# Kernel optimization log

Hardware: AMD Instinct MI355X
Metric: run time of the kernel (lower is better)

## Reference

```python
import jax, jax.numpy as jnp
import numpy as np
import math

D = 128          # domain_size (cells per side)
CELL = 0.1       # cell_size
PS = 0.1         # particle_size
KN = 6.0e6       # spring stiffness
_ALPHA = -math.log(0.5) / math.pi
_GAMMA = _ALPHA / math.sqrt(_ALPHA ** 2 + 1.0)
PM = 4.0 / 3.0 * 3.1415 * CELL ** 3 * 2700.0   # particle_mass
ETA = 2.0 * _GAMMA * math.sqrt(KN * PM)          # damping_coefficient_Eta
DT = 1e-4
EPS = 1e-4       # torch.clamp(dist, 0.0001)

# all 125 roll shifts (k-2, j-2, i-2) applied to dims (2,3,4) of a (1,1,D,D,D) field
SHIFTS = jnp.array([[k - 2, j - 2, i - 2]
                    for i in range(5) for j in range(5) for k in range(5)], dtype=jnp.int32)


def _roll3(a, sh):
    return jnp.roll(a, (sh[0], sh[1], sh[2]), axis=(2, 3, 4))


def _collision(n, xg, yg, zg, vx, vy, vz):
    """Accumulate spring-damper contact force on layer n from both layers over 125 offsets."""
    xn, yn, zn = xg[n], yg[n], zg[n]
    vxn, vyn, vzn = vx[n], vy[n], vz[n]

    def body(carry, sh):
        fx, fy, fz = carry
        for m in range(2):  # the two particle layers (diff*1 / diff*2 in the torch code)
            dx = xn - _roll3(xg[m], sh)
            dy = yn - _roll3(yg[m], sh)
            dz = zn - _roll3(zg[m], sh)
            # tiny floor inside sqrt keeps the self-offset (dist=0) finite; force there is 0 either way
            dist = jnp.sqrt(jnp.maximum(dx * dx + dy * dy + dz * dz, 1e-12))
            dc = jnp.maximum(dist, EPS)
            dvn = ((vxn - _roll3(vx[m], sh)) * dx
                   + (vyn - _roll3(vy[m], sh)) * dy
                   + (vzn - _roll3(vz[m], sh)) * dz) / dc
            # spring + normal damping, gated by overlap (dist < particle_size)
            coef = jnp.where(dist < PS, (KN * (dist - PS) + ETA * dvn) / dc, 0.0)
            fx = fx + coef * dx
            fy = fy + coef * dy
            fz = fz + coef * dz
        return (fx, fy, fz), None

    z0 = jnp.zeros((1, 1, D, D, D), jnp.float32)
    (fx, fy, fz), _ = jax.lax.scan(body, (z0, z0, z0), SHIFTS)
    return fx, fy, fz


def _boundary(p, v, m):
    lo = ((p > PS) & (p < 1.5 * PS)).astype(p.dtype)
    hi = (p > D * CELL - 0.5 * PS - CELL).astype(p.dtype)
    return (KN * lo * m * (1.5 * PS - p)
            - KN * hi * m * (p - D * CELL + CELL + 0.5 * PS)
            - ETA * v * lo * m - ETA * v * hi * m)


def _forward(x_grid, y_grid, z_grid, vx_grid, vy_grid, vz_grid, mask):
    vx, vy, vz = vx_grid, vy_grid, vz_grid
    # sequential over n: layer n=1's collision pass sees layer 0's already-updated
    # velocities, matching the in-place updates of the torch code
    for n in range(2):
        fx, fy, fz = _collision(n, x_grid, y_grid, z_grid, vx, vy, vz)
        fxb = _boundary(x_grid[n], vx[n], mask[n])
        fyb = _boundary(y_grid[n], vy[n], mask[n])
        fzb = _boundary(z_grid[n], vz[n], mask[n])
        vx = vx.at[n].set(vx[n] + DT / PM * mask[n] * (-fx + fxb))
        vy = vy.at[n].set(vy[n] + DT / PM * mask[n] * (-fy + fyb))
        vz = vz.at[n].set(vz[n] + DT / PM * mask[n] * (-9.8 * PM - fz + fzb))
    return jnp.stack([vx, vy, vz])  # (3, 2, 1, 1, D, D, D) updated velocities


def setup_inputs() -> dict:
    key = jax.random.key(0)
    ks = jax.random.split(key, 7)
    shape = (2, 1, 1, D, D, D)
    c = jnp.arange(D, dtype=jnp.float32) * CELL
    # particle position = cell corner + uniform jitter -> realistic contacts (dist < PS)
    x_grid = c[None, None, None, None, None, :] + jax.random.uniform(ks[0], shape, jnp.float32) * CELL
    y_grid = c[None, None, None, None, :, None] + jax.random.uniform(ks[1], shape, jnp.float32) * CELL
    z_grid = c[None, None, None, :, None, None] + jax.random.uniform(ks[2], shape, jnp.float32) * CELL
    vx_grid = 0.1 * jax.random.normal(ks[3], shape, jnp.float32)
    vy_grid = 0.1 * jax.random.normal(ks[4], shape, jnp.float32)
    vz_grid = 0.1 * jax.random.normal(ks[5], shape, jnp.float32)
    mask = (jax.random.uniform(ks[6], shape) < 0.5).astype(jnp.float32)  # cell occupancy
    return {"x_grid": x_grid, "y_grid": y_grid, "z_grid": z_grid,
            "vx_grid": vx_grid, "vy_grid": vy_grid, "vz_grid": vz_grid, "mask": mask}


def reference(x_grid, y_grid, z_grid, vx_grid, vy_grid, vz_grid, mask):
    return _forward(x_grid, y_grid, z_grid, vx_grid, vy_grid, vz_grid, mask)
```

## Files before the change

### kernel.cpp

```cpp
#include <hip/hip_runtime.h>
#include <math.h>

namespace {

constexpr int DD = 128;
constexpr int DM = 127;
constexpr int D3 = DD * DD * DD;

struct Consts {
  float kn, ps, eta, dtpm, grav;
  float lo_hi;
  float hi_th;
  float dcell;
  float cell;
  float hps;
  float ps2;
  float nknps;
};

__device__ inline float bforce(float p, float v, float mkv, const Consts& c) {
  float lo = ((p > c.ps) && (p < c.lo_hi)) ? mkv : 0.0f;
  float hi = (p > c.hi_th) ? mkv : 0.0f;
  float t = ((p - c.dcell) + c.cell) + c.hps;
  return c.kn * lo * (c.lo_hi - p) - c.kn * hi * t - c.eta * v * lo - c.eta * v * hi;
}

__device__ __forceinline__ float f4c(const float4& v, int u) {
  return u == 0 ? v.x : (u == 1 ? v.y : (u == 2 ? v.z : v.w));
}

template <int R>
__device__ void collide(int x, int y, int z,
                        const float* __restrict__ xg, const float* __restrict__ yg,
                        const float* __restrict__ zg,
                        const float* __restrict__ v0x, const float* __restrict__ v0y,
                        const float* __restrict__ v0z,
                        const float* __restrict__ v1x, const float* __restrict__ v1y,
                        const float* __restrict__ v1z,
                        float xn, float yn, float zn,
                        float vxn, float vyn, float vzn,
                        float& fx, float& fy, float& fz, const Consts& c) {
  int xw[2 * R + 1];
#pragma unroll
  for (int ox = -R; ox <= R; ++ox) xw[ox + R] = (x + ox) & DM;

  for (int oz = -R; oz <= R; ++oz) {
    const int zr = (z + oz) & DM;
    for (int oy = -R; oy <= R; ++oy) {
      const int yr = (y + oy) & DM;
      const int rb = (zr * DD + yr) * DD;
#pragma unroll
      for (int m = 0; m < 2; ++m) {
        const float* __restrict__ PX = xg + m * D3 + rb;
        const float* __restrict__ PY = yg + m * D3 + rb;
        const float* __restrict__ PZ = zg + m * D3 + rb;
        const float* __restrict__ VX = (m == 0 ? v0x : v1x) + rb;
        const float* __restrict__ VY = (m == 0 ? v0y : v1y) + rb;
        const float* __restrict__ VZ = (m == 0 ? v0z : v1z) + rb;
#pragma unroll
        for (int ox = -R; ox <= R; ++ox) {
          const int xi = xw[ox + R];
          float dx = xn - PX[xi];
          float dy = yn - PY[xi];
          float dz = zn - PZ[xi];
          float d2 = fmaf(dx, dx, fmaf(dy, dy, dz * dz));
          float d2c = fmaxf(d2, 1e-12f);
          float r = __builtin_amdgcn_rsqf(d2c);
          float dist = d2c * r;
          float inv = fminf(r, 1.0e4f);
          float dvx = vxn - VX[xi];
          float dvy = vyn - VY[xi];
          float dvz = vzn - VZ[xi];
          float dvn = fmaf(dvx, dx, fmaf(dvy, dy, dvz * dz)) * inv;
          float coef = (dist < c.ps) ? (fmaf(c.kn, dist - c.ps, c.eta * dvn) * inv) : 0.0f;
          fx = fmaf(coef, dx, fx);
          fy = fmaf(coef, dy, fy);
          fz = fmaf(coef, dz, fz);
        }
      }
    }
  }
}

__global__ void __launch_bounds__(256)
checker(const float* __restrict__ xg, const float* __restrict__ yg,
        const float* __restrict__ zg, unsigned* flag, float cell) {
  int i = blockIdx.x * 256 + threadIdx.x;
  int ix = i & DM;
  int iy = (i >> 7) & DM;
  int iz = (i >> 14) & DM;
  float jx = xg[i] - ix * cell;
  float jy = yg[i] - iy * cell;
  float jz = zg[i] - iz * cell;
  const float lo = -1e-5f, hi = cell + 1e-5f;
  bool bad = (jx < lo) | (jx > hi) | (jy < lo) | (jy > hi) | (jz < lo) | (jz > hi);
  if (bad) atomicOr(flag, 1u);
}

__global__ void __launch_bounds__(256)
dem_pass(int n,
         const float* __restrict__ xg, const float* __restrict__ yg,
         const float* __restrict__ zg,
         const float* __restrict__ v0x, const float* __restrict__ v0y,
         const float* __restrict__ v0z,
         const float* __restrict__ v1x, const float* __restrict__ v1y,
         const float* __restrict__ v1z,
         const float* __restrict__ vnx, const float* __restrict__ vny,
         const float* __restrict__ vnz,
         const float* __restrict__ maskn,
         float* __restrict__ outx, float* __restrict__ outy, float* __restrict__ outz,
         const unsigned* __restrict__ flag, Consts cc) {
  const int t = threadIdx.x;
  const int tx = t & 31;
  const int ty = t >> 5;
  const int wg = blockIdx.x;
  const int id = ((wg & 7) << 8) | (wg >> 3);
  const int z = id >> 4;
  const int y = ((id & 15) << 3) | ty;
  const int x0 = tx << 2;
  const int idx = (z * DD + y) * DD + x0;
  const int nn = n * D3;

  const float4 xc4 = *(const float4*)(xg + nn + idx);
  const float4 yc4 = *(const float4*)(yg + nn + idx);
  const float4 zc4 = *(const float4*)(zg + nn + idx);
  const float4 vx4 = *(const float4*)(vnx + idx);
  const float4 vy4 = *(const float4*)(vny + idx);
  const float4 vz4 = *(const float4*)(vnz + idx);
  const float4 mk4 = *(const float4*)(maskn + idx);

  float pxc[4] = {xc4.x, xc4.y, xc4.z, xc4.w};
  float pyc[4] = {yc4.x, yc4.y, yc4.z, yc4.w};
  float pzc[4] = {zc4.x, zc4.y, zc4.z, zc4.w};
  float vxc[4] = {vx4.x, vx4.y, vx4.z, vx4.w};
  float vyc[4] = {vy4.x, vy4.y, vy4.z, vy4.w};
  float vzc[4] = {vz4.x, vz4.y, vz4.z, vz4.w};
  float mkc[4] = {mk4.x, mk4.y, mk4.z, mk4.w};

  float fxA[4] = {0.f, 0.f, 0.f, 0.f};
  float fyA[4] = {0.f, 0.f, 0.f, 0.f};
  float fzA[4] = {0.f, 0.f, 0.f, 0.f};

  if (*flag == 0u) {
    const int laneL = (t & 32) | ((tx + 31) & 31);
    const int laneR = (t & 32) | ((tx + 1) & 31);
    const float* __restrict__ Q0[6] = {xg, yg, zg, v0x, v0y, v0z};
    const float* __restrict__ Q1[6] = {xg + D3, yg + D3, zg + D3, v1x, v1y, v1z};

    const float KNc = cc.kn, PS2 = cc.ps2, NKNPS = cc.nknps, ETAc = cc.eta;

    auto compute_row = [&](const float4 (&Bf)[6]) {
      float lo[6], hi[6];
#pragma unroll
      for (int f = 0; f < 6; ++f) {
        lo[f] = __shfl(Bf[f].w, laneL, 64);
        hi[f] = __shfl(Bf[f].x, laneR, 64);
      }
#pragma unroll
      for (int i = 0; i < 4; ++i) {
#pragma unroll
        for (int ox = 0; ox < 3; ++ox) {
          const int u = i + ox - 1;
          const float wx  = (u < 0) ? lo[0] : ((u > 3) ? hi[0] : f4c(Bf[0], u));
          const float wy  = (u < 0) ? lo[1] : ((u > 3) ? hi[1] : f4c(Bf[1], u));
          const float wz  = (u < 0) ? lo[2] : ((u > 3) ? hi[2] : f4c(Bf[2], u));
          const float wvx = (u < 0) ? lo[3] : ((u > 3) ? hi[3] : f4c(Bf[3], u));
          const float wvy = (u < 0) ? lo[4] : ((u > 3) ? hi[4] : f4c(Bf[4], u));
          const float wvz = (u < 0) ? lo[5] : ((u > 3) ? hi[5] : f4c(Bf[5], u));
          float dx = pxc[i] - wx;
          float dy = pyc[i] - wy;
          float dz = pzc[i] - wz;
          float d2 = fmaf(dx, dx, fmaf(dy, dy, dz * dz));
          float r = __builtin_amdgcn_rsqf(d2);
          float inv = fminf(r, 1.0e4f);
          float inv2 = inv * inv;
          float dvx = vxc[i] - wvx;
          float dvy = vyc[i] - wvy;
          float dvz = vzc[i] - wvz;
          float dvnr = fmaf(dvx, dx, fmaf(dvy, dy, dvz * dz));
          float coef = fmaf(ETAc, dvnr * inv2, fmaf(NKNPS, inv, KNc));
          coef = (d2 < PS2) ? coef : 0.0f;
          fxA[i] = fmaf(coef, dx, fxA[i]);
          fyA[i] = fmaf(coef, dy, fyA[i]);
          fzA[i] = fmaf(coef, dz, fzA[i]);
        }
      }
    };

    float4 A[6], B[6];
    {
      const int rb0 = (((z + DM) & DM) * DD + ((y + DM) & DM)) * DD + x0;
#pragma unroll
      for (int f = 0; f < 6; ++f) A[f] = *(const float4*)(Q0[f] + rb0);
    }

#pragma unroll 1
    for (int k = 0; k < 9; ++k) {
      const int iz = (k * 11) >> 5;
      const int iy = k - iz * 3;
      const int rb = (((z + iz + DM) & DM) * DD + ((y + iy + DM) & DM)) * DD + x0;
#pragma unroll
      for (int f = 0; f < 6; ++f) B[f] = *(const float4*)(Q1[f] + rb);
      compute_row(A);
      const int k1 = (k < 8) ? k + 1 : 8;
      const int iz1 = (k1 * 11) >> 5;
      const int iy1 = k1 - iz1 * 3;
      const int rb1 = (((z + iz1 + DM) & DM) * DD + ((y + iy1 + DM) & DM)) * DD + x0;
#pragma unroll
      for (int f = 0; f < 6; ++f) A[f] = *(const float4*)(Q0[f] + rb1);
      compute_row(B);
    }
  } else {
#pragma unroll
    for (int i = 0; i < 4; ++i) {
      collide<2>(x0 + i, y, z, xg, yg, zg, v0x, v0y, v0z, v1x, v1y, v1z,
                 pxc[i], pyc[i], pzc[i], vxc[i], vyc[i], vzc[i],
                 fxA[i], fyA[i], fzA[i], cc);
    }
  }

  float4 ox4, oy4, oz4;
#pragma unroll
  for (int i = 0; i < 4; ++i) {
    const float fxb = bforce(pxc[i], vxc[i], mkc[i], cc);
    const float fyb = bforce(pyc[i], vyc[i], mkc[i], cc);
    const float fzb = bforce(pzc[i], vzc[i], mkc[i], cc);
    const float s = cc.dtpm * mkc[i];
    (&ox4.x)[i] = vxc[i] + s * (fxb - fxA[i]);
    (&oy4.x)[i] = vyc[i] + s * (fyb - fyA[i]);
    (&oz4.x)[i] = vzc[i] + s * ((cc.grav - fzA[i]) + fzb);
  }
  *(float4*)(outx + idx) = ox4;
  *(float4*)(outy + idx) = oy4;
  *(float4*)(outz + idx) = oz4;
}

}

extern "C" void kernel_launch(void* const* d_in, const int* in_sizes, int n_in,
                              void* d_out, int out_size, void* d_ws, size_t ws_size,
                              hipStream_t stream) {
  const float* xg = (const float*)d_in[0];
  const float* yg = (const float*)d_in[1];
  const float* zg = (const float*)d_in[2];
  const float* vx = (const float*)d_in[3];
  const float* vy = (const float*)d_in[4];
  const float* vz = (const float*)d_in[5];
  const float* mk = (const float*)d_in[6];
  float* out = (float*)d_out;
  unsigned* flag = (unsigned*)d_ws;

  const double PSd = 0.1, CELLd = 0.1, KNd = 6.0e6;
  const double ALPHA = -log(0.5) / 3.141592653589793;
  const double GAMMA = ALPHA / sqrt(ALPHA * ALPHA + 1.0);
  const double PMd = 4.0 / 3.0 * 3.1415 * (0.1 * 0.1 * 0.1) * 2700.0;
  const double ETAd = 2.0 * GAMMA * sqrt(KNd * PMd);

  Consts cc;
  cc.kn = (float)KNd;
  cc.ps = (float)PSd;
  cc.eta = (float)ETAd;
  cc.dtpm = (float)(1e-4 / PMd);
  cc.grav = (float)(-9.8 * PMd);
  cc.lo_hi = (float)(1.5 * PSd);
  cc.hi_th = (float)(DD * CELLd - 0.5 * PSd - CELLd);
  cc.dcell = (float)(DD * CELLd);
  cc.cell = (float)CELLd;
  cc.hps = (float)(0.5 * PSd);
  cc.ps2 = cc.ps * cc.ps;
  cc.nknps = -(cc.kn * cc.ps);

  hipMemsetAsync(d_ws, 0, sizeof(unsigned), stream);
  checker<<<(2 * D3) / 256, 256, 0, stream>>>(xg, yg, zg, flag, cc.cell);

  dim3 blk(256, 1, 1), grd(2048, 1, 1);
  dem_pass<<<grd, blk, 0, stream>>>(
      0, xg, yg, zg,
      vx, vy, vz,
      vx + D3, vy + D3, vz + D3,
      vx, vy, vz,
      mk,
      out, out + 2 * D3, out + 4 * D3,
      flag, cc);
  dem_pass<<<grd, blk, 0, stream>>>(
      1, xg, yg, zg,
      out, out + 2 * D3, out + 4 * D3,
      vx + D3, vy + D3, vz + D3,
      vx + D3, vy + D3, vz + D3,
      mk + D3,
      out + D3, out + 3 * D3, out + 5 * D3,
      flag, cc);
}
```

Before: 192.5 us.

## Register-block two y-rows per thread to share neighbor row loads

Each thread now computes two adjacent y rows instead of one. It walks 12 neighbor rows (3 z by 4 y) instead of 9 and applies each loaded row to both output rows where it is in range. This cuts global and L2 loads per output from 9 rows to 6, and the grid is halved to match. The cost is more live registers, which may lower occupancy, and half as many workgroups.

```diff
diff --git a/kernel.cpp b/kernel.cpp
--- a/kernel.cpp
+++ b/kernel.cpp
@@ -114,32 +114,36 @@
   const int tx = t & 31;
   const int ty = t >> 5;
   const int wg = blockIdx.x;
-  const int id = ((wg & 7) << 8) | (wg >> 3);
-  const int z = id >> 4;
-  const int y = ((id & 15) << 3) | ty;
+  const int id = ((wg & 7) << 7) | (wg >> 3);
+  const int z = id >> 3;
+  const int y0 = ((id & 7) << 4) | (ty << 1);
   const int x0 = tx << 2;
-  const int idx = (z * DD + y) * DD + x0;
+  const int idx0 = (z * DD + y0) * DD + x0;
+  const int idx1 = idx0 + DD;
   const int nn = n * D3;
 
-  const float4 xc4 = *(const float4*)(xg + nn + idx);
-  const float4 yc4 = *(const float4*)(yg + nn + idx);
-  const float4 zc4 = *(const float4*)(zg + nn + idx);
-  const float4 vx4 = *(const float4*)(vnx + idx);
-  const float4 vy4 = *(const float4*)(vny + idx);
-  const float4 vz4 = *(const float4*)(vnz + idx);
-  const float4 mk4 = *(const float4*)(maskn + idx);
-
-  float pxc[4] = {xc4.x, xc4.y, xc4.z, xc4.w};
-  float pyc[4] = {yc4.x, yc4.y, yc4.z, yc4.w};
-  float pzc[4] = {zc4.x, zc4.y, zc4.z, zc4.w};
-  float vxc[4] = {vx4.x, vx4.y, vx4.z, vx4.w};
-  float vyc[4] = {vy4.x, vy4.y, vy4.z, vy4.w};
-  float vzc[4] = {vz4.x, vz4.y, vz4.z, vz4.w};
-  float mkc[4] = {mk4.x, mk4.y, mk4.z, mk4.w};
-
-  float fxA[4] = {0.f, 0.f, 0.f, 0.f};
-  float fyA[4] = {0.f, 0.f, 0.f, 0.f};
-  float fzA[4] = {0.f, 0.f, 0.f, 0.f};
+  float px0[4], py0[4], pz0[4], vx0[4], vy0[4], vz0[4], mk0[4];
+  float px1[4], py1[4], pz1[4], vx1[4], vy1[4], vz1[4], mk1[4];
+  {
+    float4 a;
+    a = *(const float4*)(xg + nn + idx0);  px0[0]=a.x; px0[1]=a.y; px0[2]=a.z; px0[3]=a.w;
+    a = *(const float4*)(yg + nn + idx0);  py0[0]=a.x; py0[1]=a.y; py0[2]=a.z; py0[3]=a.w;
+    a = *(const float4*)(zg + nn + idx0);  pz0[0]=a.x; pz0[1]=a.y; pz0[2]=a.z; pz0[3]=a.w;
+    a = *(const float4*)(vnx + idx0);      vx0[0]=a.x; vx0[1]=a.y; vx0[2]=a.z; vx0[3]=a.w;
+    a = *(const float4*)(vny + idx0);      vy0[0]=a.x; vy0[1]=a.y; vy0[2]=a.z; vy0[3]=a.w;
+    a = *(const float4*)(vnz + idx0);      vz0[0]=a.x; vz0[1]=a.y; vz0[2]=a.z; vz0[3]=a.w;
+    a = *(const float4*)(maskn + idx0);    mk0[0]=a.x; mk0[1]=a.y; mk0[2]=a.z; mk0[3]=a.w;
+    a = *(const float4*)(xg + nn + idx1);  px1[0]=a.x; px1[1]=a.y; px1[2]=a.z; px1[3]=a.w;
+    a = *(const float4*)(yg + nn + idx1);  py1[0]=a.x; py1[1]=a.y; py1[2]=a.z; py1[3]=a.w;
+    a = *(const float4*)(zg + nn + idx1);  pz1[0]=a.x; pz1[1]=a.y; pz1[2]=a.z; pz1[3]=a.w;
+    a = *(const float4*)(vnx + idx1);      vx1[0]=a.x; vx1[1]=a.y; vx1[2]=a.z; vx1[3]=a.w;
+    a = *(const float4*)(vny + idx1);      vy1[0]=a.x; vy1[1]=a.y; vy1[2]=a.z; vy1[3]=a.w;
+    a = *(const float4*)(vnz + idx1);      vz1[0]=a.x; vz1[1]=a.y; vz1[2]=a.z; vz1[3]=a.w;
+    a = *(const float4*)(maskn + idx1);    mk1[0]=a.x; mk1[1]=a.y; mk1[2]=a.z; mk1[3]=a.w;
+  }
+
+  float fx0[4] = {0.f,0.f,0.f,0.f}, fy0[4] = {0.f,0.f,0.f,0.f}, fz0[4] = {0.f,0.f,0.f,0.f};
+  float fx1[4] = {0.f,0.f,0.f,0.f}, fy1[4] = {0.f,0.f,0.f,0.f}, fz1[4] = {0.f,0.f,0.f,0.f};
 
   if (*flag == 0u) {
     const int laneL = (t & 32) | ((tx + 31) & 31);
@@ -149,90 +153,116 @@
 
     const float KNc = cc.kn, PS2 = cc.ps2, NKNPS = cc.nknps, ETAc = cc.eta;
 
-    auto compute_row = [&](const float4 (&Bf)[6]) {
-      float lo[6], hi[6];
-#pragma unroll
-      for (int f = 0; f < 6; ++f) {
-        lo[f] = __shfl(Bf[f].w, laneL, 64);
-        hi[f] = __shfl(Bf[f].x, laneR, 64);
-      }
+    auto interact4 = [&](const float4 (&Rf)[6], const float (&lo)[6], const float (&hi)[6],
+                         const float (&px)[4], const float (&py)[4], const float (&pz)[4],
+                         const float (&vx)[4], const float (&vy)[4], const float (&vz)[4],
+                         float (&fx)[4], float (&fy)[4], float (&fz)[4]) {
 #pragma unroll
       for (int i = 0; i < 4; ++i) {
 #pragma unroll
         for (int ox = 0; ox < 3; ++ox) {
           const int u = i + ox - 1;
-          const float wx  = (u < 0) ? lo[0] : ((u > 3) ? hi[0] : f4c(Bf[0], u));
-          const float wy  = (u < 0) ? lo[1] : ((u > 3) ? hi[1] : f4c(Bf[1], u));
-          const float wz  = (u < 0) ? lo[2] : ((u > 3) ? hi[2] : f4c(Bf[2], u));
-          const float wvx = (u < 0) ? lo[3] : ((u > 3) ? hi[3] : f4c(Bf[3], u));
-          const float wvy = (u < 0) ? lo[4] : ((u > 3) ? hi[4] : f4c(Bf[4], u));
-          const float wvz = (u < 0) ? lo[5] : ((u > 3) ? hi[5] : f4c(Bf[5], u));
-          float dx = pxc[i] - wx;
-          float dy = pyc[i] - wy;
-          float dz = pzc[i] - wz;
+          const float wx  = (u < 0) ? lo[0] : ((u > 3) ? hi[0] : f4c(Rf[0], u));
+          const float wy  = (u < 0) ? lo[1] : ((u > 3) ? hi[1] : f4c(Rf[1], u));
+          const float wz  = (u < 0) ? lo[2] : ((u > 3) ? hi[2] : f4c(Rf[2], u));
+          const float wvx = (u < 0) ? lo[3] : ((u > 3) ? hi[3] : f4c(Rf[3], u));
+          const float wvy = (u < 0) ? lo[4] : ((u > 3) ? hi[4] : f4c(Rf[4], u));
+          const float wvz = (u < 0) ? lo[5] : ((u > 3) ? hi[5] : f4c(Rf[5], u));
+          float dx = px[i] - wx;
+          float dy = py[i] - wy;
+          float dz = pz[i] - wz;
           float d2 = fmaf(dx, dx, fmaf(dy, dy, dz * dz));
           float r = __builtin_amdgcn_rsqf(d2);
           float inv = fminf(r, 1.0e4f);
           float inv2 = inv * inv;
-          float dvx = vxc[i] - wvx;
-          float dvy = vyc[i] - wvy;
-          float dvz = vzc[i] - wvz;
+          float dvx = vx[i] - wvx;
+          float dvy = vy[i] - wvy;
+          float dvz = vz[i] - wvz;
           float dvnr = fmaf(dvx, dx, fmaf(dvy, dy, dvz * dz));
           float coef = fmaf(ETAc, dvnr * inv2, fmaf(NKNPS, inv, KNc));
           coef = (d2 < PS2) ? coef : 0.0f;
-          fxA[i] = fmaf(coef, dx, fxA[i]);
-          fyA[i] = fmaf(coef, dy, fyA[i]);
-          fzA[i] = fmaf(coef, dz, fzA[i]);
+          fx[i] = fmaf(coef, dx, fx[i]);
+          fy[i] = fmaf(coef, dy, fy[i]);
+          fz[i] = fmaf(coef, dz, fz[i]);
         }
       }
     };
 
+    auto compute_row = [&](const float4 (&Rf)[6], int j) {
+      float lo[6], hi[6];
+#pragma unroll
+      for (int f = 0; f < 6; ++f) {
+        lo[f] = __shfl(Rf[f].w, laneL, 64);
+        hi[f] = __shfl(Rf[f].x, laneR, 64);
+      }
+      if (j != 3) interact4(Rf, lo, hi, px0, py0, pz0, vx0, vy0, vz0, fx0, fy0, fz0);
+      if (j != 0) interact4(Rf, lo, hi, px1, py1, pz1, vx1, vy1, vz1, fx1, fy1, fz1);
+    };
+
+    auto rowbase = [&](int k) -> int {
+      const int zr = (z + (k >> 2) + DM) & DM;
+      const int yr = (y0 + (k & 3) + DM) & DM;
+      return (zr * DD + yr) * DD + x0;
+    };
+
     float4 A[6], B[6];
     {
-      const int rb0 = (((z + DM) & DM) * DD + ((y + DM) & DM)) * DD + x0;
+      const int rb0 = rowbase(0);
 #pragma unroll
       for (int f = 0; f < 6; ++f) A[f] = *(const float4*)(Q0[f] + rb0);
     }
 
 #pragma unroll 1
-    for (int k = 0; k < 9; ++k) {
-      const int iz = (k * 11) >> 5;
-      const int iy = k - iz * 3;
-      const int rb = (((z + iz + DM) & DM) * DD + ((y + iy + DM) & DM)) * DD + x0;
+    for (int k = 0; k < 12; ++k) {
+      const int j = k & 3;
+      const int rb = rowbase(k);
 #pragma unroll
       for (int f = 0; f < 6; ++f) B[f] = *(const float4*)(Q1[f] + rb);
-      compute_row(A);
-      const int k1 = (k < 8) ? k + 1 : 8;
-      const int iz1 = (k1 * 11) >> 5;
-      const int iy1 = k1 - iz1 * 3;
-      const int rb1 = (((z + iz1 + DM) & DM) * DD + ((y + iy1 + DM) & DM)) * DD + x0;
+      compute_row(A, j);
+      const int rb1 = rowbase(k < 11 ? k + 1 : 11);
 #pragma unroll
       for (int f = 0; f < 6; ++f) A[f] = *(const float4*)(Q0[f] + rb1);
-      compute_row(B);
+      compute_row(B, j);
     }
   } else {
 #pragma unroll
     for (int i = 0; i < 4; ++i) {
-      collide<2>(x0 + i, y, z, xg, yg, zg, v0x, v0y, v0z, v1x, v1y, v1z,
-                 pxc[i], pyc[i], pzc[i], vxc[i], vyc[i], vzc[i],
-                 fxA[i], fyA[i], fzA[i], cc);
+      collide<2>(x0 + i, y0, z, xg, yg, zg, v0x, v0y, v0z, v1x, v1y, v1z,
+                 px0[i], py0[i], pz0[i], vx0[i], vy0[i], vz0[i],
+                 fx0[i], fy0[i], fz0[i], cc);
+      collide<2>(x0 + i, y0 + 1, z, xg, yg, zg, v0x, v0y, v0z, v1x, v1y, v1z,
+                 px1[i], py1[i], pz1[i], vx1[i], vy1[i], vz1[i],
+                 fx1[i], fy1[i], fz1[i], cc);
     }
   }
 
   float4 ox4, oy4, oz4;
 #pragma unroll
   for (int i = 0; i < 4; ++i) {
-    const float fxb = bforce(pxc[i], vxc[i], mkc[i], cc);
-    const float fyb = bforce(pyc[i], vyc[i], mkc[i], cc);
-    const float fzb = bforce(pzc[i], vzc[i], mkc[i], cc);
-    const float s = cc.dtpm * mkc[i];
-    (&ox4.x)[i] = vxc[i] + s * (fxb - fxA[i]);
-    (&oy4.x)[i] = vyc[i] + s * (fyb - fyA[i]);
-    (&oz4.x)[i] = vzc[i] + s * ((cc.grav - fzA[i]) + fzb);
-  }
-  *(float4*)(outx + idx) = ox4;
-  *(float4*)(outy + idx) = oy4;
-  *(float4*)(outz + idx) = oz4;
+    const float fxb = bforce(px0[i], vx0[i], mk0[i], cc);
+    const float fyb = bforce(py0[i], vy0[i], mk0[i], cc);
+    const float fzb = bforce(pz0[i], vz0[i], mk0[i], cc);
+    const float s = cc.dtpm * mk0[i];
+    (&ox4.x)[i] = vx0[i] + s * (fxb - fx0[i]);
+    (&oy4.x)[i] = vy0[i] + s * (fyb - fy0[i]);
+    (&oz4.x)[i] = vz0[i] + s * ((cc.grav - fz0[i]) + fzb);
+  }
+  *(float4*)(outx + idx0) = ox4;
+  *(float4*)(outy + idx0) = oy4;
+  *(float4*)(outz + idx0) = oz4;
+#pragma unroll
+  for (int i = 0; i < 4; ++i) {
+    const float fxb = bforce(px1[i], vx1[i], mk1[i], cc);
+    const float fyb = bforce(py1[i], vy1[i], mk1[i], cc);
+    const float fzb = bforce(pz1[i], vz1[i], mk1[i], cc);
+    const float s = cc.dtpm * mk1[i];
+    (&ox4.x)[i] = vx1[i] + s * (fxb - fx1[i]);
+    (&oy4.x)[i] = vy1[i] + s * (fyb - fy1[i]);
+    (&oz4.x)[i] = vz1[i] + s * ((cc.grav - fz1[i]) + fzb);
+  }
+  *(float4*)(outx + idx1) = ox4;
+  *(float4*)(outy + idx1) = oy4;
+  *(float4*)(outz + idx1) = oz4;
 }
 
 }
@@ -273,7 +303,7 @@
   hipMemsetAsync(d_ws, 0, sizeof(unsigned), stream);
   checker<<<(2 * D3) / 256, 256, 0, stream>>>(xg, yg, zg, flag, cc.cell);
 
-  dim3 blk(256, 1, 1), grd(2048, 1, 1);
+  dim3 blk(256, 1, 1), grd(1024, 1, 1);
   dem_pass<<<grd, blk, 0, stream>>>(
       0, xg, yg, zg,
       vx, vy, vz,
```

Result: faster. 176.4 us (-8.3%).
